# Performance work log

Hardware: AMD Instinct MI355X
Metric: run time of the kernel (lower is better)

The kernel has to match this reference:

```python
import jax, jax.numpy as jnp
import numpy as np

N_NODES = 50000
N_EDGES = 600000
IN_CH = 128
HID = 128   # 2 * out_channels
OUT_CH = 64


def setup_inputs() -> dict:
    key = jax.random.key(0)
    ks = jax.random.split(key, 5)
    x = jax.random.normal(ks[0], (N_NODES, IN_CH), dtype=jnp.float32)
    edge_index = jax.random.randint(ks[1], (2, N_EDGES), 0, N_NODES, dtype=jnp.int64)
    # Glorot-style init for the GCNConv linear weights
    W1 = jax.random.normal(ks[2], (IN_CH, HID), dtype=jnp.float32) * (1.0 / np.sqrt(IN_CH))
    b1 = jnp.zeros((HID,), dtype=jnp.float32)
    W2 = jax.random.normal(ks[3], (HID, OUT_CH), dtype=jnp.float32) * (1.0 / np.sqrt(HID))
    b2 = jnp.zeros((OUT_CH,), dtype=jnp.float32)
    return {"x": x, "edge_index": edge_index, "W1": W1, "b1": b1, "W2": W2, "b2": b2}


def reference(x, edge_index, W1, b1, W2, b2):
    N = x.shape[0]
    # --- GCN normalization with self-loops (cached: computed once, shared by both layers) ---
    loop = jnp.arange(N, dtype=edge_index.dtype)
    src = jnp.concatenate([edge_index[0], loop])   # [E+N]
    dst = jnp.concatenate([edge_index[1], loop])   # [E+N]
    deg = jax.ops.segment_sum(jnp.ones_like(src, dtype=x.dtype), dst, num_segments=N)
    d_inv_sqrt = jnp.where(deg > 0, jax.lax.rsqrt(deg), 0.0)
    norm = d_inv_sqrt[src] * d_inv_sqrt[dst]       # [E+N] edge weights of D^-1/2 (A+I) D^-1/2

    def gcn_conv(h, W, b):
        h = h @ W                                   # dense transform first (PyG GCNConv)
        msg = h[src] * norm[:, None]                # gather + scale per edge
        agg = jax.ops.segment_sum(msg, dst, num_segments=N)  # scatter-add to dst nodes
        return agg + b

    h = jax.nn.relu(gcn_conv(x, W1, b1))
    return gcn_conv(h, W2, b2)
```

## Files before the change

### kernel.cpp

```cpp
#include <hip/hip_runtime.h>


constexpr int IN_CH  = 128;
constexpr int HID    = 128;
constexpr int OUT_CH = 64;
constexpr int PAD    = 128;
constexpr int KSTR   = 40;

using short8v = __attribute__((ext_vector_type(8))) short;
using f32x4v  = __attribute__((ext_vector_type(4))) float;

__device__ __forceinline__ unsigned short f2bf_rne(float f) {
    unsigned int u = __float_as_uint(f);
    u += 0x7FFFu + ((u >> 16) & 1u);
    return (unsigned short)(u >> 16);
}
__device__ __forceinline__ float bf2f(unsigned short h) {
    return __uint_as_float((unsigned int)h << 16);
}

__device__ __forceinline__ bool probe_is64(const int* __restrict__ ei) {
    const int v = ei[2 * (threadIdx.x & 63) + 1];
    return __ballot(v != 0) == 0ull;
}

__device__ __forceinline__ void load_idx4(const int* __restrict__ ei, bool is64,
                                          long long hb, int e0, int n, int* out) {
    const long long p = hb + e0;
    if (is64) {
        if (n == 4 && ((p & 1) == 0)) {
            const int4 a = *reinterpret_cast<const int4*>(ei + 2 * p);
            const int4 b = *reinterpret_cast<const int4*>(ei + 2 * p + 4);
            out[0] = a.x; out[1] = a.z; out[2] = b.x; out[3] = b.z;
        } else {
            for (int j = 0; j < n; ++j) out[j] = ei[2 * (p + j)];
        }
    } else {
        if (n == 4 && ((p & 3) == 0)) {
            const int4 a = *reinterpret_cast<const int4*>(ei + p);
            out[0] = a.x; out[1] = a.y; out[2] = a.z; out[3] = a.w;
        } else {
            for (int j = 0; j < n; ++j) out[j] = ei[p + j];
        }
    }
}

__global__ __launch_bounds__(256) void k_init(int* __restrict__ cursor, int N,
                                              const float* __restrict__ W1,
                                              const float* __restrict__ W2,
                                              unsigned short* __restrict__ w1th,
                                              unsigned short* __restrict__ w1tl,
                                              unsigned short* __restrict__ w2th,
                                              unsigned short* __restrict__ w2tl) {
    const int b = blockIdx.x;
    if (b < 64) {
        const int i = b * 256 + threadIdx.x;
        const int n4 = N / 4;
        for (int j = i; j < n4; j += 64 * 256)
            reinterpret_cast<int4*>(cursor)[j] = make_int4(0, 0, 0, 0);
        const int tail = n4 * 4 + i;
        if (tail < N) cursor[tail] = 0;
    } else if (b < 80) {
        const int i = (b - 64) * 1024 + threadIdx.x * 4;
        const int n = i >> 7, k = i & 127;
#pragma unroll
        for (int j = 0; j < 4; ++j) {
            const float f = W1[(size_t)(k + j) * HID + n];
            const unsigned short h = f2bf_rne(f);
            w1th[n * 128 + k + j] = h;
            w1tl[n * 128 + k + j] = f2bf_rne(f - bf2f(h));
        }
    } else {
        const int i = (b - 80) * 1024 + threadIdx.x * 4;
        const int n = i >> 7, k = i & 127;
#pragma unroll
        for (int j = 0; j < 4; ++j) {
            const float f = W2[(size_t)(k + j) * OUT_CH + n];
            const unsigned short h = f2bf_rne(f);
            w2th[n * 128 + k + j] = h;
            w2tl[n * 128 + k + j] = f2bf_rne(f - bf2f(h));
        }
    }
}

__device__ __forceinline__ void gemm1_mfma_lds(
    const float* __restrict__ X, const unsigned short* __restrict__ w1th,
    const unsigned short* __restrict__ w1tl, unsigned short* __restrict__ Y,
    int M, int blk) {
    __shared__ __align__(16) unsigned short lh[128 * KSTR];
    __shared__ __align__(16) unsigned short ll[128 * KSTR];

    const int tid = threadIdx.x;
    const int wv  = tid >> 6;
    const int ln  = tid & 63;
    const int m16 = ln & 15;
    const int g   = ln >> 4;
    const int arow = blk * 64 + wv * 16 + m16;

    f32x4v acc[8];
#pragma unroll
    for (int n = 0; n < 8; ++n) acc[n] = {0.f, 0.f, 0.f, 0.f};

    for (int k0 = 0; k0 < 128; k0 += 32) {
        __syncthreads();
#pragma unroll
        for (int q = 0; q < 4; ++q) {
            const int id = tid + q * 256;
            if (id < 512) {
                const int n = id >> 2, c = id & 3;
                *reinterpret_cast<short8v*>(&lh[n * KSTR + c * 8]) =
                    *reinterpret_cast<const short8v*>(w1th + n * 128 + k0 + c * 8);
            } else {
                const int id2 = id - 512;
                const int n = id2 >> 2, c = id2 & 3;
                *reinterpret_cast<short8v*>(&ll[n * KSTR + c * 8]) =
                    *reinterpret_cast<const short8v*>(w1tl + n * 128 + k0 + c * 8);
            }
        }
        __syncthreads();

        short8v ah, al;
        if (arow < M) {
            const float4 a0 = *reinterpret_cast<const float4*>(
                X + (size_t)arow * 128 + k0 + g * 8);
            const float4 a1 = *reinterpret_cast<const float4*>(
                X + (size_t)arow * 128 + k0 + g * 8 + 4);
            const float f[8] = {a0.x, a0.y, a0.z, a0.w, a1.x, a1.y, a1.z, a1.w};
#pragma unroll
            for (int e = 0; e < 8; ++e) {
                const unsigned short h = f2bf_rne(f[e]);
                ah[e] = (short)h;
                al[e] = (short)f2bf_rne(f[e] - bf2f(h));
            }
        } else {
#pragma unroll
            for (int e = 0; e < 8; ++e) { ah[e] = 0; al[e] = 0; }
        }

#pragma unroll
        for (int n = 0; n < 8; ++n) {
            const short8v bh = *reinterpret_cast<const short8v*>(
                &lh[(n * 16 + m16) * KSTR + g * 8]);
            const short8v bl = *reinterpret_cast<const short8v*>(
                &ll[(n * 16 + m16) * KSTR + g * 8]);
            acc[n] = __builtin_amdgcn_mfma_f32_16x16x32_bf16(ah, bh, acc[n], 0, 0, 0);
            acc[n] = __builtin_amdgcn_mfma_f32_16x16x32_bf16(al, bh, acc[n], 0, 0, 0);
            acc[n] = __builtin_amdgcn_mfma_f32_16x16x32_bf16(ah, bl, acc[n], 0, 0, 0);
        }
    }

#pragma unroll
    for (int r = 0; r < 4; ++r) {
        const int orow = blk * 64 + wv * 16 + g * 4 + r;
        if (orow < M) {
#pragma unroll
            for (int n = 0; n < 8; ++n)
                Y[(size_t)orow * 128 + n * 16 + m16] = f2bf_rne(acc[n][r]);
        }
    }
}

__global__ __launch_bounds__(256) void k_gemm1_fill(
    const float* __restrict__ X, const unsigned short* __restrict__ w1th,
    const unsigned short* __restrict__ w1tl, unsigned short* __restrict__ Y,
    int M, int gemmBlocks, const int* __restrict__ ei,
    int* __restrict__ cursor, unsigned short* __restrict__ csr16, int E) {
    if ((int)blockIdx.x < gemmBlocks) {
        gemm1_mfma_lds(X, w1th, w1tl, Y, M, blockIdx.x);
        return;
    }
    const bool is64 = probe_is64(ei);
    const int nthr = (gridDim.x - gemmBlocks) * 256;
    const int idx  = (blockIdx.x - gemmBlocks) * 256 + threadIdx.x;
    for (int e0 = idx * 4; e0 < E; e0 += nthr * 4) {
        const int n = min(4, E - e0);
        int s[4], d[4];
        load_idx4(ei, is64, 0,            e0, n, s);
        load_idx4(ei, is64, (long long)E, e0, n, d);
        int r[4];
        for (int j = 0; j < n; ++j) r[j] = atomicAdd(&cursor[d[j]], 1);
        for (int j = 0; j < n; ++j)
            if (r[j] < PAD)
                csr16[((size_t)d[j] << 7) + r[j]] = (unsigned short)s[j];
    }
}

__global__ void k_dinv(const int* __restrict__ cursor, float* __restrict__ dinv, int N) {
    int i = blockIdx.x * blockDim.x + threadIdx.x;
    for (; i < N; i += gridDim.x * blockDim.x)
        dinv[i] = rsqrtf((float)(cursor[i] + 1));
}

__global__ __launch_bounds__(256) void k_gather_relu(
    const unsigned short* __restrict__ h, const int* __restrict__ deg,
    const unsigned short* __restrict__ csr16, const float* __restrict__ dinv,
    const float* __restrict__ b, unsigned short* __restrict__ aggb, int N) {
    constexpr int LPN = HID / 4;
    const int tid  = blockIdx.x * blockDim.x + threadIdx.x;
    const int node = tid / LPN;
    const int lane = tid % LPN;
    if (node >= N) return;

    const float dn = dinv[node];
    float4 acc = reinterpret_cast<const float4*>(b)[lane];
    {
        const float w = dn * dn;
        const ushort4 v = *reinterpret_cast<const ushort4*>(h + (size_t)node * HID + lane * 4);
        acc.x = fmaf(bf2f(v.x), w, acc.x); acc.y = fmaf(bf2f(v.y), w, acc.y);
        acc.z = fmaf(bf2f(v.z), w, acc.z); acc.w = fmaf(bf2f(v.w), w, acc.w);
    }

    const unsigned short* row = csr16 + ((size_t)node << 7);
    int dg = deg[node];
    if (dg > PAD) dg = PAD;
    int e = 0;
    for (; e + 1 < dg; e += 2) {
        const int s0 = row[e];
        const int s1 = row[e + 1];
        const float w0 = dinv[s0] * dn;
        const float w1 = dinv[s1] * dn;
        const ushort4 v0 = *reinterpret_cast<const ushort4*>(h + (size_t)s0 * HID + lane * 4);
        const ushort4 v1 = *reinterpret_cast<const ushort4*>(h + (size_t)s1 * HID + lane * 4);
        acc.x = fmaf(bf2f(v0.x), w0, acc.x); acc.y = fmaf(bf2f(v0.y), w0, acc.y);
        acc.z = fmaf(bf2f(v0.z), w0, acc.z); acc.w = fmaf(bf2f(v0.w), w0, acc.w);
        acc.x = fmaf(bf2f(v1.x), w1, acc.x); acc.y = fmaf(bf2f(v1.y), w1, acc.y);
        acc.z = fmaf(bf2f(v1.z), w1, acc.z); acc.w = fmaf(bf2f(v1.w), w1, acc.w);
    }
    if (e < dg) {
        const int s0 = row[e];
        const float w0 = dinv[s0] * dn;
        const ushort4 v0 = *reinterpret_cast<const ushort4*>(h + (size_t)s0 * HID + lane * 4);
        acc.x = fmaf(bf2f(v0.x), w0, acc.x); acc.y = fmaf(bf2f(v0.y), w0, acc.y);
        acc.z = fmaf(bf2f(v0.z), w0, acc.z); acc.w = fmaf(bf2f(v0.w), w0, acc.w);
    }

    ushort4 o;
    o.x = f2bf_rne(fmaxf(acc.x, 0.f));
    o.y = f2bf_rne(fmaxf(acc.y, 0.f));
    o.z = f2bf_rne(fmaxf(acc.z, 0.f));
    o.w = f2bf_rne(fmaxf(acc.w, 0.f));
    *reinterpret_cast<ushort4*>(aggb + (size_t)node * HID + lane * 4) = o;
}

__global__ __launch_bounds__(256) void k_gemm2_mfma(
    const unsigned short* __restrict__ Xb, const unsigned short* __restrict__ w2th,
    const unsigned short* __restrict__ w2tl, unsigned short* __restrict__ Y, int M) {
    const int tid = threadIdx.x;
    const int wv  = tid >> 6;
    const int ln  = tid & 63;
    const int m16 = ln & 15;
    const int g   = ln >> 4;
    const int arow = blockIdx.x * 64 + wv * 16 + m16;

    f32x4v acc[4];
#pragma unroll
    for (int n = 0; n < 4; ++n) acc[n] = {0.f, 0.f, 0.f, 0.f};

#pragma unroll
    for (int k0 = 0; k0 < 128; k0 += 32) {
        short8v a;
        if (arow < M) {
            a = *reinterpret_cast<const short8v*>(Xb + (size_t)arow * 128 + k0 + g * 8);
        } else {
#pragma unroll
            for (int e = 0; e < 8; ++e) a[e] = 0;
        }
#pragma unroll
        for (int n = 0; n < 4; ++n) {
            const short8v bh = *reinterpret_cast<const short8v*>(
                w2th + (n * 16 + m16) * 128 + k0 + g * 8);
            const short8v bl = *reinterpret_cast<const short8v*>(
                w2tl + (n * 16 + m16) * 128 + k0 + g * 8);
            acc[n] = __builtin_amdgcn_mfma_f32_16x16x32_bf16(a, bh, acc[n], 0, 0, 0);
            acc[n] = __builtin_amdgcn_mfma_f32_16x16x32_bf16(a, bl, acc[n], 0, 0, 0);
        }
    }

#pragma unroll
    for (int r = 0; r < 4; ++r) {
        const int orow = blockIdx.x * 64 + wv * 16 + g * 4 + r;
        if (orow < M) {
#pragma unroll
            for (int n = 0; n < 4; ++n)
                Y[(size_t)orow * 64 + n * 16 + m16] = f2bf_rne(acc[n][r]);
        }
    }
}

__global__ __launch_bounds__(256) void k_gather64(
    const unsigned short* __restrict__ h, const int* __restrict__ deg,
    const unsigned short* __restrict__ csr16, const float* __restrict__ dinv,
    const float* __restrict__ b, float* __restrict__ out, int N) {
    constexpr int LPN = OUT_CH / 4;
    const int tid  = blockIdx.x * blockDim.x + threadIdx.x;
    const int node = tid / LPN;
    const int lane = tid % LPN;
    if (node >= N) return;

    const float dn = dinv[node];
    float4 acc = reinterpret_cast<const float4*>(b)[lane];
    {
        const float w = dn * dn;
        const ushort4 v = *reinterpret_cast<const ushort4*>(h + (size_t)node * OUT_CH + lane * 4);
        acc.x = fmaf(bf2f(v.x), w, acc.x); acc.y = fmaf(bf2f(v.y), w, acc.y);
        acc.z = fmaf(bf2f(v.z), w, acc.z); acc.w = fmaf(bf2f(v.w), w, acc.w);
    }

    const unsigned short* row = csr16 + ((size_t)node << 7);
    int dg = deg[node];
    if (dg > PAD) dg = PAD;
    int e = 0;
    for (; e + 1 < dg; e += 2) {
        const int s0 = row[e];
        const int s1 = row[e + 1];
        const float w0 = dinv[s0] * dn;
        const float w1 = dinv[s1] * dn;
        const ushort4 v0 = *reinterpret_cast<const ushort4*>(h + (size_t)s0 * OUT_CH + lane * 4);
        const ushort4 v1 = *reinterpret_cast<const ushort4*>(h + (size_t)s1 * OUT_CH + lane * 4);
        acc.x = fmaf(bf2f(v0.x), w0, acc.x); acc.y = fmaf(bf2f(v0.y), w0, acc.y);
        acc.z = fmaf(bf2f(v0.z), w0, acc.z); acc.w = fmaf(bf2f(v0.w), w0, acc.w);
        acc.x = fmaf(bf2f(v1.x), w1, acc.x); acc.y = fmaf(bf2f(v1.y), w1, acc.y);
        acc.z = fmaf(bf2f(v1.z), w1, acc.z); acc.w = fmaf(bf2f(v1.w), w1, acc.w);
    }
    if (e < dg) {
        const int s0 = row[e];
        const float w0 = dinv[s0] * dn;
        const ushort4 v0 = *reinterpret_cast<const ushort4*>(h + (size_t)s0 * OUT_CH + lane * 4);
        acc.x = fmaf(bf2f(v0.x), w0, acc.x); acc.y = fmaf(bf2f(v0.y), w0, acc.y);
        acc.z = fmaf(bf2f(v0.z), w0, acc.z); acc.w = fmaf(bf2f(v0.w), w0, acc.w);
    }

    reinterpret_cast<float4*>(out + (size_t)node * OUT_CH)[lane] = acc;
}

extern "C" void kernel_launch(void* const* d_in, const int* in_sizes, int n_in,
                              void* d_out, int out_size, void* d_ws, size_t ws_size,
                              hipStream_t stream) {
    const float* x  = (const float*)d_in[0];
    const int*   ei = (const int*)d_in[1];
    const float* W1 = (const float*)d_in[2];
    const float* b1 = (const float*)d_in[3];
    const float* W2 = (const float*)d_in[4];
    const float* b2 = (const float*)d_in[5];
    float* out = (float*)d_out;

    const int N = in_sizes[0] / IN_CH;
    const int E = in_sizes[1] / 2;

    char* wsb = (char*)d_ws;
    size_t off = 0;
    auto alloc = [&](size_t bytes) -> void* {
        void* p = wsb + off;
        off += (bytes + 255) & ~(size_t)255;
        return p;
    };
    int*   cursor = (int*)alloc((size_t)N * sizeof(int));
    float* dinv   = (float*)alloc((size_t)N * sizeof(float));
    unsigned short* w1th  = (unsigned short*)alloc(128 * 128 * sizeof(unsigned short));
    unsigned short* w1tl  = (unsigned short*)alloc(128 * 128 * sizeof(unsigned short));
    unsigned short* w2th  = (unsigned short*)alloc(64 * 128 * sizeof(unsigned short));
    unsigned short* w2tl  = (unsigned short*)alloc(64 * 128 * sizeof(unsigned short));
    unsigned short* csr16 = (unsigned short*)alloc((size_t)N * PAD * sizeof(unsigned short));
    unsigned short* h1b   = (unsigned short*)alloc((size_t)N * HID * sizeof(unsigned short));
    unsigned short* aggb  = (unsigned short*)alloc((size_t)N * HID * sizeof(unsigned short));
    unsigned short* h2b   = (unsigned short*)alloc((size_t)N * OUT_CH * sizeof(unsigned short));

    auto gs = [](long long n) { return (int)((n + 255) / 256); };

    k_init<<<88, 256, 0, stream>>>(cursor, N, W1, W2, w1th, w1tl, w2th, w2tl);

    const int gemmBlocks = (N + 63) / 64;
    const int fillBlocks = 512;
    k_gemm1_fill<<<gemmBlocks + fillBlocks, 256, 0, stream>>>(
        x, w1th, w1tl, h1b, N, gemmBlocks, ei, cursor, csr16, E);

    k_dinv<<<gs(N), 256, 0, stream>>>(cursor, dinv, N);

    k_gather_relu<<<gs((long long)N * (HID / 4)), 256, 0, stream>>>(
        h1b, cursor, csr16, dinv, b1, aggb, N);

    k_gemm2_mfma<<<(N + 63) / 64, 256, 0, stream>>>(aggb, w2th, w2tl, h2b, N);

    k_gather64<<<gs((long long)N * (OUT_CH / 4)), 256, 0, stream>>>(
        h2b, cursor, csr16, dinv, b2, out, N);
}
```

Before: 117.4 us.

## Build CSR via two-pass bucketed fill with LDS-local degree counting

New measurement: 182.7 us. 55.6% more time.

```diff
diff --git a/kernel.cpp b/kernel.cpp
--- a/kernel.cpp
+++ b/kernel.cpp
@@ -6,6 +6,8 @@
 constexpr int OUT_CH = 64;
 constexpr int PAD    = 128;
 constexpr int KSTR   = 40;
+constexpr int SB     = 8;
+constexpr int BCAP   = 768;
 
 using short8v = __attribute__((ext_vector_type(8))) short;
 using f32x4v  = __attribute__((ext_vector_type(4))) float;
@@ -45,7 +47,7 @@
     }
 }
 
-__global__ __launch_bounds__(256) void k_init(int* __restrict__ cursor, int N,
+__global__ __launch_bounds__(256) void k_init(int* __restrict__ bcur, int nbk,
                                               const float* __restrict__ W1,
                                               const float* __restrict__ W2,
                                               unsigned short* __restrict__ w1th,
@@ -53,15 +55,10 @@
                                               unsigned short* __restrict__ w2th,
                                               unsigned short* __restrict__ w2tl) {
     const int b = blockIdx.x;
-    if (b < 64) {
-        const int i = b * 256 + threadIdx.x;
-        const int n4 = N / 4;
-        for (int j = i; j < n4; j += 64 * 256)
-            reinterpret_cast<int4*>(cursor)[j] = make_int4(0, 0, 0, 0);
-        const int tail = n4 * 4 + i;
-        if (tail < N) cursor[tail] = 0;
-    } else if (b < 80) {
-        const int i = (b - 64) * 1024 + threadIdx.x * 4;
+    if (b == 0) {
+        for (int i = threadIdx.x; i < nbk; i += 256) bcur[i] = 0;
+    } else if (b < 17) {
+        const int i = (b - 1) * 1024 + threadIdx.x * 4;
         const int n = i >> 7, k = i & 127;
 #pragma unroll
         for (int j = 0; j < 4; ++j) {
@@ -71,7 +68,7 @@
             w1tl[n * 128 + k + j] = f2bf_rne(f - bf2f(h));
         }
     } else {
-        const int i = (b - 80) * 1024 + threadIdx.x * 4;
+        const int i = (b - 17) * 1024 + threadIdx.x * 4;
         const int n = i >> 7, k = i & 127;
 #pragma unroll
         for (int j = 0; j < 4; ++j) {
@@ -160,11 +157,11 @@
     }
 }
 
-__global__ __launch_bounds__(256) void k_gemm1_fill(
+__global__ __launch_bounds__(256) void k_gemm1_fillA(
     const float* __restrict__ X, const unsigned short* __restrict__ w1th,
     const unsigned short* __restrict__ w1tl, unsigned short* __restrict__ Y,
     int M, int gemmBlocks, const int* __restrict__ ei,
-    int* __restrict__ cursor, unsigned short* __restrict__ csr16, int E) {
+    int* __restrict__ bcur, unsigned int* __restrict__ bbuf, int E) {
     if ((int)blockIdx.x < gemmBlocks) {
         gemm1_mfma_lds(X, w1th, w1tl, Y, M, blockIdx.x);
         return;
@@ -172,23 +169,55 @@
     const bool is64 = probe_is64(ei);
     const int nthr = (gridDim.x - gemmBlocks) * 256;
     const int idx  = (blockIdx.x - gemmBlocks) * 256 + threadIdx.x;
+    const int sub  = threadIdx.x & (SB - 1);
     for (int e0 = idx * 4; e0 < E; e0 += nthr * 4) {
         const int n = min(4, E - e0);
         int s[4], d[4];
         load_idx4(ei, is64, 0,            e0, n, s);
         load_idx4(ei, is64, (long long)E, e0, n, d);
-        int r[4];
-        for (int j = 0; j < n; ++j) r[j] = atomicAdd(&cursor[d[j]], 1);
+        int b[4], pos[4];
+        for (int j = 0; j < n; ++j) b[j] = ((d[j] >> 8) << 3) | sub;
+        for (int j = 0; j < n; ++j) pos[j] = atomicAdd(&bcur[b[j]], 1);
         for (int j = 0; j < n; ++j)
-            if (r[j] < PAD)
-                csr16[((size_t)d[j] << 7) + r[j]] = (unsigned short)s[j];
-    }
-}
-
-__global__ void k_dinv(const int* __restrict__ cursor, float* __restrict__ dinv, int N) {
-    int i = blockIdx.x * blockDim.x + threadIdx.x;
-    for (; i < N; i += gridDim.x * blockDim.x)
-        dinv[i] = rsqrtf((float)(cursor[i] + 1));
+            if (pos[j] < BCAP)
+                bbuf[(size_t)b[j] * BCAP + pos[j]] =
+                    ((unsigned int)(d[j] & 255) << 16) | (unsigned int)s[j];
+    }
+}
+
+__global__ __launch_bounds__(256) void k_fillB(
+    const int* __restrict__ bcur, const unsigned int* __restrict__ bbuf,
+    unsigned short* __restrict__ csr16, int* __restrict__ indeg,
+    float* __restrict__ dinv, int N) {
+    __shared__ int cnt[256];
+    const int tid = threadIdx.x;
+    const int rb  = blockIdx.x;
+    cnt[tid] = 0;
+    __syncthreads();
+
+    const int base = rb << 8;
+#pragma unroll
+    for (int sb = 0; sb < SB; ++sb) {
+        const int bk = (rb << 3) | sb;
+        int c = bcur[bk];
+        if (c > BCAP) c = BCAP;
+        const unsigned int* buf = bbuf + (size_t)bk * BCAP;
+        for (int i = tid; i < c; i += 256) {
+            const unsigned int e = buf[i];
+            const int dlow = (int)(e >> 16);
+            const int s    = (int)(e & 0xffffu);
+            const int r = atomicAdd(&cnt[dlow], 1);
+            if (r < PAD)
+                csr16[(((size_t)(base + dlow)) << 7) + r] = (unsigned short)s;
+        }
+    }
+    __syncthreads();
+    const int node = base + tid;
+    if (node < N) {
+        const int dg = cnt[tid];
+        indeg[node] = dg;
+        dinv[node]  = rsqrtf((float)(dg + 1));
+    }
 }
 
 __global__ __launch_bounds__(256) void k_gather_relu(
@@ -344,8 +373,10 @@
     const float* b2 = (const float*)d_in[5];
     float* out = (float*)d_out;
 
-    const int N = in_sizes[0] / IN_CH;
-    const int E = in_sizes[1] / 2;
+    const int N   = in_sizes[0] / IN_CH;
+    const int E   = in_sizes[1] / 2;
+    const int NR  = (N + 255) >> 8;
+    const int NBK = NR * SB;
 
     char* wsb = (char*)d_ws;
     size_t off = 0;
@@ -354,8 +385,10 @@
         off += (bytes + 255) & ~(size_t)255;
         return p;
     };
-    int*   cursor = (int*)alloc((size_t)N * sizeof(int));
-    float* dinv   = (float*)alloc((size_t)N * sizeof(float));
+    int*   bcur  = (int*)alloc((size_t)NBK * sizeof(int));
+    int*   indeg = (int*)alloc((size_t)N * sizeof(int));
+    float* dinv  = (float*)alloc((size_t)N * sizeof(float));
+    unsigned int* bbuf = (unsigned int*)alloc((size_t)NBK * BCAP * sizeof(unsigned int));
     unsigned short* w1th  = (unsigned short*)alloc(128 * 128 * sizeof(unsigned short));
     unsigned short* w1tl  = (unsigned short*)alloc(128 * 128 * sizeof(unsigned short));
     unsigned short* w2th  = (unsigned short*)alloc(64 * 128 * sizeof(unsigned short));
@@ -367,20 +400,20 @@
 
     auto gs = [](long long n) { return (int)((n + 255) / 256); };
 
-    k_init<<<88, 256, 0, stream>>>(cursor, N, W1, W2, w1th, w1tl, w2th, w2tl);
+    k_init<<<25, 256, 0, stream>>>(bcur, NBK, W1, W2, w1th, w1tl, w2th, w2tl);
 
     const int gemmBlocks = (N + 63) / 64;
     const int fillBlocks = 512;
-    k_gemm1_fill<<<gemmBlocks + fillBlocks, 256, 0, stream>>>(
-        x, w1th, w1tl, h1b, N, gemmBlocks, ei, cursor, csr16, E);
-
-    k_dinv<<<gs(N), 256, 0, stream>>>(cursor, dinv, N);
+    k_gemm1_fillA<<<gemmBlocks + fillBlocks, 256, 0, stream>>>(
+        x, w1th, w1tl, h1b, N, gemmBlocks, ei, bcur, bbuf, E);
+
+    k_fillB<<<NR, 256, 0, stream>>>(bcur, bbuf, csr16, indeg, dinv, N);
 
     k_gather_relu<<<gs((long long)N * (HID / 4)), 256, 0, stream>>>(
-        h1b, cursor, csr16, dinv, b1, aggb, N);
+        h1b, indeg, csr16, dinv, b1, aggb, N);
 
     k_gemm2_mfma<<<(N + 63) / 64, 256, 0, stream>>>(aggb, w2th, w2tl, h2b, N);
 
     k_gather64<<<gs((long long)N * (OUT_CH / 4)), 256, 0, stream>>>(
-        h2b, cursor, csr16, dinv, b2, out, N);
-}
+        h2b, indeg, csr16, dinv, b2, out, N);
+}
```
